# Optimization experiments

Measured on AMD Instinct MI355X. Metric: run time of the kernel, lower is better.

Reference implementation:

```python
import jax, jax.numpy as jnp
import numpy as np

B, H = 1, 512
NVAR, NCLS = 16384, 65536
NP, NM = 4096, 4096
NEG = -1e30


def setup_inputs() -> dict:
    key = jax.random.key(0)
    ks = jax.random.split(key, 16)
    s = 0.02  # weight init scale
    return {
        "literal_emb": jax.random.normal(ks[0], (B, 2 * NVAR, H), jnp.float32),
        "clause_emb": jax.random.normal(ks[1], (B, NCLS, H), jnp.float32),
        "pos_idx": jax.random.randint(ks[2], (NP,), 0, NCLS),
        "neg_idx": jax.random.randint(ks[3], (NM,), 0, NCLS),
        "keep_mask": jax.random.randint(ks[4], (NP, NM), 0, 2).astype(bool),
        "taken_mask": jax.random.uniform(ks[5], (NP, NM)) < 0.01,  # sparse exclusion set
        "var_K_w": s * jax.random.normal(ks[6], (H, H), jnp.float32),
        "var_K_b": jnp.zeros((H,), jnp.float32),
        "var_Q_w": s * jax.random.normal(ks[7], (H, H), jnp.float32),
        "var_Q_b": jnp.zeros((H,), jnp.float32),
        "var_attn_w": s * jax.random.normal(ks[8], (1, H), jnp.float32),
        "var_attn_b": jnp.zeros((1,), jnp.float32),
        "W_Q_w": s * jax.random.normal(ks[9], (H, H), jnp.float32),
        "W_Q_b": jnp.zeros((H,), jnp.float32),
        "W_K_w": s * jax.random.normal(ks[10], (H, H), jnp.float32),
        "W_K_b": jnp.zeros((H,), jnp.float32),
    }


def reference(literal_emb, clause_emb, pos_idx, neg_idx, keep_mask, taken_mask,
              var_K_w, var_K_b, var_Q_w, var_Q_b, var_attn_w, var_attn_b,
              W_Q_w, W_Q_b, W_K_w, W_K_b):
    n_vars = literal_emb.shape[1] // 2
    # --- select_var: additive attention over positive literals ---
    K = literal_emb[:, :n_vars]                       # [B, V, H]
    K_t = K @ var_K_w.T + var_K_b                     # [B, V, H]
    Q = clause_emb.sum(axis=1)                        # [B, H] (C_aggr='sum')
    Q_t = Q @ var_Q_w.T + var_Q_b                     # [B, H]
    u = (jnp.tanh(K_t + Q_t[:, None, :]) @ var_attn_w.T + var_attn_b)[..., 0]  # [B, V]
    log_score = jax.nn.log_softmax(u, axis=-1)
    var_logp = jnp.max(log_score, axis=-1)            # [B]
    var_idx = jnp.argmax(log_score, axis=-1)          # [B]
    # --- clause-pair attention over pivot pos/neg clause pools ---
    q = clause_emb[:, pos_idx] @ W_Q_w.T + W_Q_b      # [B, NP, H]
    k = clause_emb[:, neg_idx] @ W_K_w.T + W_K_b      # [B, NM, H]
    h = q.shape[-1]
    scores = jnp.einsum('bnh,bmh->bnm', q, k) / jnp.sqrt(jnp.float32(h))
    # mask_grid_asym: drop invalid (keep_mask==0) and already-taken pairs, log-normalize
    valid = keep_mask & (~taken_mask)                 # [NP, NM]
    masked = jnp.where(valid[None], scores, jnp.float32(NEG))
    flat = masked.reshape(masked.shape[0], -1)        # [B, NP*NM]
    logp = jax.nn.log_softmax(flat, axis=-1)
    C_logp = jnp.max(logp, axis=-1)                   # [B]
    C_flat = jnp.argmax(logp, axis=-1)                # [B]
    M = scores.shape[-1]
    ci, cj = C_flat // M, C_flat % M
    c_idx_pos = pos_idx[ci]                           # map back to global clause ids
    c_idx_neg = neg_idx[cj]
    c_logp = C_logp + var_logp                        # [B]
    return (c_logp, c_idx_pos, c_idx_neg, var_idx)
```

## Files before the change

### kernel.cpp

```cpp
#include <hip/hip_runtime.h>
#include <hip/hip_bf16.h>
#include <math.h>

#define HH 512
#define NVARS 16384
#define NPOS 4096
#define NMS 4096
#define NEGV -1.0e30f
#define RSQRT_H 0.04419417382415922f

#define BM 128
#define BK 16

typedef unsigned short u16;
typedef __attribute__((ext_vector_type(8))) short bf16x8;
typedef __attribute__((ext_vector_type(4))) float f32x4;

struct SPart { float m; float s; int a; int pad; };

__device__ inline u16 f2bf(float f) {
  unsigned u = __float_as_uint(f);
  unsigned r = (u + 0x7fffu + ((u >> 16) & 1u)) >> 16;
  return (u16)r;
}
__device__ inline float bf2f(u16 h) { return __uint_as_float(((unsigned)h) << 16); }

__device__ inline void wreduce_maxidx(float& v, int& idx) {
#pragma unroll
  for (int m = 1; m < 64; m <<= 1) {
    float ov = __shfl_xor(v, m, 64);
    int oi = __shfl_xor(idx, m, 64);
    if (ov > v || (ov == v && oi < idx)) { v = ov; idx = oi; }
  }
}

__device__ inline float wreduce_sum(float v) {
#pragma unroll
  for (int m = 1; m < 64; m <<= 1) v += __shfl_xor(v, m, 64);
  return v;
}

__device__ __forceinline__ void stage_frag(const u16* src, u16* dst) {
  __builtin_amdgcn_global_load_lds(
      (const __attribute__((address_space(1))) void*)src,
      (__attribute__((address_space(3))) void*)dst, 16, 0, 0);
}

__global__ __launch_bounds__(256) void pack_kernel(
    const void* __restrict__ keep, const void* __restrict__ taken,
    unsigned long long* __restrict__ vmask) {
  __shared__ unsigned char nib[256];
  const unsigned* kw = (const unsigned*)keep;
  int f = 1;
#pragma unroll
  for (int i = 0; i < 16; ++i) f &= (kw[i] <= 1u);
  const int t = threadIdx.x;
  const size_t e = (size_t)blockIdx.x * 1024 + (size_t)t * 4;
  int v0, v1, v2, v3;
  if (f) {
    uint4 kv = *(const uint4*)((const unsigned int*)keep + e);
    uint4 tv = *(const uint4*)((const unsigned int*)taken + e);
    v0 = kv.x && !tv.x; v1 = kv.y && !tv.y; v2 = kv.z && !tv.z; v3 = kv.w && !tv.w;
  } else {
    unsigned kv = *(const unsigned*)((const unsigned char*)keep + e);
    unsigned tv = *(const unsigned*)((const unsigned char*)taken + e);
    v0 = (kv & 0xffu) && !(tv & 0xffu);
    v1 = (kv & 0xff00u) && !(tv & 0xff00u);
    v2 = (kv & 0xff0000u) && !(tv & 0xff0000u);
    v3 = (kv & 0xff000000u) && !(tv & 0xff000000u);
  }
  nib[t] = (unsigned char)(v0 | (v1 << 1) | (v2 << 2) | (v3 << 3));
  __syncthreads();
  if (t < 16) {
    unsigned long long m = 0;
#pragma unroll
    for (int j = 0; j < 16; ++j)
      m |= (unsigned long long)nib[t * 16 + j] << (4 * j);
    vmask[(size_t)blockIdx.x * 16 + t] = m;
  }
}

__global__ __launch_bounds__(256) void qsum_kernel(
    const float* __restrict__ clause, double* __restrict__ qpart) {
  const int b = blockIdx.x, t = threadIdx.x;
  const int fg = t & 127;
  const int rh = t >> 7;
  const float* base = clause + (size_t)(b * 128 + rh * 64) * HH + fg * 4;
  double a0 = 0.0, a1 = 0.0, a2 = 0.0, a3 = 0.0;
#pragma unroll 4
  for (int r = 0; r < 64; ++r) {
    float4 v = *(const float4*)(base + (size_t)r * HH);
    a0 += (double)v.x; a1 += (double)v.y; a2 += (double)v.z; a3 += (double)v.w;
  }
  double* o = qpart + (size_t)(b * 2 + rh) * HH + fg * 4;
  o[0] = a0; o[1] = a1; o[2] = a2; o[3] = a3;
}

__global__ __launch_bounds__(256) void qred_kernel(
    const double* __restrict__ qpart, double* __restrict__ Qd) {
  __shared__ double red[256];
  const int t = threadIdx.x;
  const int h = blockIdx.x * 16 + (t & 15);
  const int chunk = t >> 4;
  double s = 0.0;
  for (int j = 0; j < 64; ++j) s += qpart[(size_t)(chunk * 64 + j) * HH + h];
  red[t] = s;
  __syncthreads();
  for (int off = 8; off > 0; off >>= 1) {
    if (chunk < off) red[t] += red[t + off * 16];
    __syncthreads();
  }
  if (t < 16) Qd[blockIdx.x * 16 + t] = red[t];
}

__global__ __launch_bounds__(256) void prepmv_kernel(
    const double* __restrict__ Qd, const float* __restrict__ varQw,
    const float* __restrict__ varQb, const float* __restrict__ varKb,
    float* __restrict__ tvec) {
  __shared__ double red[256];
  const int t = threadIdx.x;
  const int h = blockIdx.x * 16 + (t & 15);
  const int chunk = t >> 4;
  const float* wrow = varQw + (size_t)h * HH + chunk * 32;
  const double* qd = Qd + chunk * 32;
  double s = 0.0;
  for (int j = 0; j < 32; ++j) s += qd[j] * (double)wrow[j];
  red[t] = s;
  __syncthreads();
  for (int off = 8; off > 0; off >>= 1) {
    if (chunk < off) red[t] += red[t + off * 16];
    __syncthreads();
  }
  if (t < 16) {
    int hh = blockIdx.x * 16 + t;
    tvec[hh] = (float)(red[t] + (double)varQb[hh] + (double)varKb[hh]);
  }
}

__global__ __launch_bounds__(256) void tofrag_kernel(
    const float* __restrict__ src, u16* __restrict__ hi, u16* __restrict__ lo) {
  const int frag = blockIdx.x * 4 + (threadIdx.x >> 6);
  const int lane = threadIdx.x & 63;
  const int R = frag >> 4, K = frag & 15;
  const float* p = src + (size_t)(R * 16 + (lane & 15)) * HH + K * 32 + (lane >> 4) * 8;
  float v[8];
  *(float4*)&v[0] = *(const float4*)p;
  *(float4*)&v[4] = *(const float4*)(p + 4);
  u16 h[8], l[8];
#pragma unroll
  for (int e = 0; e < 8; ++e) { h[e] = f2bf(v[e]); l[e] = f2bf(v[e] - bf2f(h[e])); }
  size_t base = (size_t)frag * 512 + (size_t)lane * 8;
  *(ushort4*)(hi + base) = *(ushort4*)&h[0];
  *(ushort4*)(hi + base + 4) = *(ushort4*)&h[4];
  *(ushort4*)(lo + base) = *(ushort4*)&l[0];
  *(ushort4*)(lo + base + 4) = *(ushort4*)&l[4];
}

#define MFMA16(A, B)                                                                 \
  _Pragma("unroll") for (int i_ = 0; i_ < 4; ++i_)                                   \
  _Pragma("unroll") for (int j_ = 0; j_ < 4; ++j_)                                   \
    acc[i_][j_] = __builtin_amdgcn_mfma_f32_16x16x32_bf16(A[i_], B[j_], acc[i_][j_], 0, 0, 0);

#define MFMAS(AH, AL, BH, BL)                                                        \
  do { MFMA16(AH, BH) MFMA16(AH, BL) MFMA16(AL, BH) } while (0)

__global__ __launch_bounds__(256, 3) void proj_kernel(
    const float* __restrict__ clause,
    const int* __restrict__ pos_idx, const int* __restrict__ neg_idx,
    const u16* __restrict__ wqhi, const u16* __restrict__ wqlo,
    const u16* __restrict__ wkhi2, const u16* __restrict__ wklo2,
    const float* __restrict__ bQ, const float* __restrict__ bK,
    float* __restrict__ qmat, float* __restrict__ kmat) {
  const int* __restrict__ idx = blockIdx.z ? neg_idx : pos_idx;
  const u16* __restrict__ bhp = blockIdx.z ? wkhi2 : wqhi;
  const u16* __restrict__ blp = blockIdx.z ? wklo2 : wqlo;
  const float* __restrict__ bias = blockIdx.z ? bK : bQ;
  float* __restrict__ out = blockIdx.z ? kmat : qmat;

  const int t = threadIdx.x, lane = t & 63, wid = t >> 6;
  const int wn = wid & 1, wm = wid >> 1;
  const int row0 = blockIdx.x * 128;
  const int col0 = blockIdx.y * 128;

  const float* aptr[4];
#pragma unroll
  for (int f = 0; f < 4; ++f) {
    int g = idx[row0 + wn * 64 + f * 16 + (lane & 15)];
    aptr[f] = clause + (size_t)g * HH + (lane >> 4) * 8;
  }
  const size_t bbase = (size_t)((col0 >> 4) + wm * 4) * 8192 + (size_t)lane * 8;

  f32x4 acc[4][4] = {};
#pragma unroll
  for (int s = 0; s < 16; ++s) {
    float rA[4][8];
    bf16x8 aH[4], aL[4], bH[4], bL[4];
#pragma unroll
    for (int f = 0; f < 4; ++f) {
      *(float4*)&rA[f][0] = *(const float4*)(aptr[f] + s * 32);
      *(float4*)&rA[f][4] = *(const float4*)(aptr[f] + s * 32 + 4);
      size_t ob = bbase + (size_t)f * 8192 + (size_t)s * 512;
      bH[f] = *(const bf16x8*)(bhp + ob);
      bL[f] = *(const bf16x8*)(blp + ob);
    }
#pragma unroll
    for (int f = 0; f < 4; ++f)
#pragma unroll
      for (int e = 0; e < 8; ++e) {
        float v = rA[f][e];
        u16 h = f2bf(v);
        aH[f][e] = (short)h;
        aL[f][e] = (short)f2bf(v - bf2f(h));
      }
    MFMAS(aH, aL, bH, bL);
  }

#pragma unroll
  for (int i = 0; i < 4; ++i)
#pragma unroll
    for (int j = 0; j < 4; ++j) {
      int h = col0 + wm * 64 + j * 16 + (lane & 15);
      float b = bias[h];
#pragma unroll
      for (int r = 0; r < 4; ++r) {
        int n = row0 + wn * 64 + i * 16 + (lane >> 4) * 4 + r;
        out[(size_t)n * HH + h] = acc[i][j][r] + b;
      }
    }
}


__global__ __launch_bounds__(256, 2) void ktu_kernel(
    const u16* __restrict__ lithi, const u16* __restrict__ litlo,
    const u16* __restrict__ wkhi, const u16* __restrict__ wklo,
    const float* __restrict__ tvec, const float* __restrict__ attnw,
    float* __restrict__ upart) {
  __shared__ __align__(16) u16 lds[2][4][8][512];
  const int t = threadIdx.x, lane = t & 63, wid = t >> 6;
  const int wn = wid & 1, wm = wid >> 1;
  const int row0 = blockIdx.x * 128;
  const int l8 = lane * 8;

  const u16* sa = (wid == 0) ? lithi : (wid == 1) ? litlo : (wid == 2) ? wkhi : wklo;
  const int rb = (wid < 2) ? (row0 >> 4) : (blockIdx.y * 8);
  const u16* sab = sa + (size_t)rb * 8192 + l8;

#define KSTAGE(buf, s)                                                        \
  _Pragma("unroll") for (int f_ = 0; f_ < 8; ++f_)                            \
    stage_frag(sab + (size_t)f_ * 8192 + (size_t)(s) * 512,                   \
               &lds[buf][wid][f_][0]);

  KSTAGE(0, 0)
  f32x4 acc[4][4] = {};
#pragma unroll
  for (int s = 0; s < 16; ++s) {
    __syncthreads();
    if (s < 15) { KSTAGE((s + 1) & 1, s + 1) }
    const int b = s & 1;
    bf16x8 aH[4], aL[4], bH[4], bL[4];
#pragma unroll
    for (int f = 0; f < 4; ++f) {
      aH[f] = *(const bf16x8*)&lds[b][0][wn * 4 + f][l8];
      aL[f] = *(const bf16x8*)&lds[b][1][wn * 4 + f][l8];
      bH[f] = *(const bf16x8*)&lds[b][2][wm * 4 + f][l8];
      bL[f] = *(const bf16x8*)&lds[b][3][wm * 4 + f][l8];
    }
    MFMAS(aH, aL, bH, bL);
  }
#undef KSTAGE

  const int cbase = blockIdx.y * 128 + wm * 64;
  float tv[4], aw[4];
#pragma unroll
  for (int j = 0; j < 4; ++j) {
    int c = cbase + j * 16 + (lane & 15);
    tv[j] = tvec[c]; aw[j] = attnw[c];
  }
  float us[4][4];
#pragma unroll
  for (int i = 0; i < 4; ++i)
#pragma unroll
    for (int r = 0; r < 4; ++r) {
      float s = 0.f;
#pragma unroll
      for (int j = 0; j < 4; ++j) {
        float x = acc[i][j][r] + tv[j];
        float th = 1.0f - 2.0f / (__expf(2.0f * x) + 1.0f);
        s += th * aw[j];
      }
      us[i][r] = s;
    }
#pragma unroll
  for (int m = 1; m < 16; m <<= 1)
#pragma unroll
    for (int i = 0; i < 4; ++i)
#pragma unroll
      for (int r = 0; r < 4; ++r) us[i][r] += __shfl_xor(us[i][r], m, 64);
  if ((lane & 15) == 0) {
#pragma unroll
    for (int i = 0; i < 4; ++i)
#pragma unroll
      for (int r = 0; r < 4; ++r) {
        int row = row0 + wn * 64 + i * 16 + (lane >> 4) * 4 + r;
        upart[(size_t)(blockIdx.y * 2 + wm) * NVARS + row] = us[i][r];
      }
  }
}

__global__ __launch_bounds__(256, 2) void scores_kernel(
    const u16* __restrict__ qhi, const u16* __restrict__ qlo,
    const u16* __restrict__ khi, const u16* __restrict__ klo,
    const unsigned long long* __restrict__ vmask, SPart* __restrict__ parts) {
  __shared__ __align__(16) u16 lds[2][4][8][512];
  __shared__ unsigned long long mrow[128][2];
  __shared__ float s_rv[4]; __shared__ int s_ri[4]; __shared__ float s_rs[4];
  __shared__ float s_bm; __shared__ int s_ba;

  const int t = threadIdx.x;
  const int lane = t & 63;
  const int wid = t >> 6;
  const int wn = wid & 1, wm = wid >> 1;
  const int l8 = lane * 8;

  const int bid = blockIdx.x;
  const int xcd = bid & 7, p = bid >> 3;
  const int sp = p >> 6, q = p & 63;
  const int g = xcd * 2 + sp;
  const int bx = (g & 3) * 8 + (q & 7);
  const int by = (g >> 2) * 8 + (q >> 3);

  const int n0 = by * 128;
  const int m0 = bx * 128;

  const u16* sa = (wid == 0) ? qhi : (wid == 1) ? qlo : (wid == 2) ? khi : klo;
  const int rb = (wid < 2) ? (n0 >> 4) : (m0 >> 4);
  const u16* sab = sa + (size_t)rb * 8192 + l8;

#define SSTAGE(buf, s)                                                        \
  _Pragma("unroll") for (int f_ = 0; f_ < 8; ++f_)                            \
    stage_frag(sab + (size_t)f_ * 8192 + (size_t)(s) * 512,                   \
               &lds[buf][wid][f_][0]);

  {
    int r = t >> 1, w = t & 1;
    mrow[r][w] = vmask[(size_t)(n0 + r) * (NMS / 64) + (m0 >> 6) + w];
  }

  SSTAGE(0, 0)
  f32x4 acc[4][4] = {};
#pragma unroll
  for (int s = 0; s < 16; ++s) {
    __syncthreads();
    if (s < 15) { SSTAGE((s + 1) & 1, s + 1) }
    const int b = s & 1;
    bf16x8 aH[4], aL[4], bH[4], bL[4];
#pragma unroll
    for (int f = 0; f < 4; ++f) {
      aH[f] = *(const bf16x8*)&lds[b][0][wn * 4 + f][l8];
      aL[f] = *(const bf16x8*)&lds[b][1][wn * 4 + f][l8];
      bH[f] = *(const bf16x8*)&lds[b][2][wm * 4 + f][l8];
      bL[f] = *(const bf16x8*)&lds[b][3][wm * 4 + f][l8];
    }
    MFMAS(aH, aL, bH, bL);
  }
#undef SSTAGE

  const int rbase = wn * 64 + (lane >> 4) * 4;
  const int cb15 = (lane & 15);

  float mv = NEGV; int mi = 0x7fffffff;
#pragma unroll
  for (int i = 0; i < 4; ++i) {
#pragma unroll
    for (int r = 0; r < 4; ++r) {
      int rl = rbase + i * 16 + r;
      unsigned long long ww = mrow[rl][wm];
      int gb = (n0 + rl) * NMS + m0;
#pragma unroll
      for (int j = 0; j < 4; ++j) {
        int bit = j * 16 + cb15;
        int cl = wm * 64 + bit;
        float sv = acc[i][j][r] * RSQRT_H;
        acc[i][j][r] = sv;
        bool valid = ((ww >> bit) & 1ull) != 0;
        if (valid && (sv > mv || (sv == mv && gb + cl < mi))) { mv = sv; mi = gb + cl; }
      }
    }
  }
  wreduce_maxidx(mv, mi);
  if ((t & 63) == 0) { s_rv[wid] = mv; s_ri[wid] = mi; }
  __syncthreads();
  if (t == 0) {
    float bm = s_rv[0]; int ba = s_ri[0];
    for (int w = 1; w < 4; ++w)
      if (s_rv[w] > bm || (s_rv[w] == bm && s_ri[w] < ba)) { bm = s_rv[w]; ba = s_ri[w]; }
    s_bm = bm; s_ba = ba;
  }
  __syncthreads();
  const float bm = s_bm;

  float se = 0.f;
#pragma unroll
  for (int i = 0; i < 4; ++i) {
#pragma unroll
    for (int r = 0; r < 4; ++r) {
      int rl = rbase + i * 16 + r;
      unsigned long long ww = mrow[rl][wm];
#pragma unroll
      for (int j = 0; j < 4; ++j) {
        int bit = j * 16 + cb15;
        bool valid = ((ww >> bit) & 1ull) != 0;
        if (valid) se += __expf(acc[i][j][r] - bm);
      }
    }
  }
  se = wreduce_sum(se);
  if ((t & 63) == 0) s_rs[wid] = se;
  __syncthreads();
  if (t == 0) {
    SPart pt;
    pt.m = s_bm;
    pt.s = s_rs[0] + s_rs[1] + s_rs[2] + s_rs[3];
    pt.a = s_ba; pt.pad = 0;
    parts[by * 32 + bx] = pt;
  }
}

__global__ __launch_bounds__(256) void usum_kernel(
    const float* __restrict__ upart, SPart* __restrict__ uparts2) {
  __shared__ float s_rv[4]; __shared__ int s_ri[4]; __shared__ float s_rs[4];
  __shared__ float s_bm; __shared__ int s_ba;
  const int t = threadIdx.x;
  const int i = blockIdx.x * 256 + t;
  float u = 0.f;
#pragma unroll
  for (int p = 0; p < 8; ++p) u += upart[(size_t)p * NVARS + i];
  float mv = u; int mi = i;
  wreduce_maxidx(mv, mi);
  if ((t & 63) == 0) { s_rv[t >> 6] = mv; s_ri[t >> 6] = mi; }
  __syncthreads();
  if (t == 0) {
    float bm = s_rv[0]; int ba = s_ri[0];
    for (int w = 1; w < 4; ++w)
      if (s_rv[w] > bm || (s_rv[w] == bm && s_ri[w] < ba)) { bm = s_rv[w]; ba = s_ri[w]; }
    s_bm = bm; s_ba = ba;
  }
  __syncthreads();
  float se = __expf(u - s_bm);
  se = wreduce_sum(se);
  if ((t & 63) == 0) s_rs[t >> 6] = se;
  __syncthreads();
  if (t == 0) {
    SPart p;
    p.m = s_bm;
    p.s = s_rs[0] + s_rs[1] + s_rs[2] + s_rs[3];
    p.a = s_ba; p.pad = 0;
    uparts2[blockIdx.x] = p;
  }
}

__global__ __launch_bounds__(256) void final_kernel(
    const SPart* __restrict__ uparts2, const SPart* __restrict__ parts,
    const int* __restrict__ pos_idx, const int* __restrict__ neg_idx,
    float* __restrict__ out) {
  __shared__ float s_rv[4]; __shared__ int s_ri[4]; __shared__ float s_rs[4];
  __shared__ float s_umax; __shared__ int s_uarg; __shared__ float s_usum;
  __shared__ float s_gm; __shared__ int s_ga;
  const int t = threadIdx.x;

  float mv = -3.0e38f; int mi = 0x7fffffff;
  SPart up;
  if (t < 64) {
    up = uparts2[t];
    mv = up.m; mi = up.a;
  }
  wreduce_maxidx(mv, mi);
  if ((t & 63) == 0) { s_rv[t >> 6] = mv; s_ri[t >> 6] = mi; }
  __syncthreads();
  if (t == 0) {
    float bm = s_rv[0]; int ba = s_ri[0];
    for (int w = 1; w < 4; ++w)
      if (s_rv[w] > bm || (s_rv[w] == bm && s_ri[w] < ba)) { bm = s_rv[w]; ba = s_ri[w]; }
    s_umax = bm; s_uarg = ba;
  }
  __syncthreads();
  float se = (t < 64) ? up.s * __expf(up.m - s_umax) : 0.f;
  se = wreduce_sum(se);
  if ((t & 63) == 0) s_rs[t >> 6] = se;
  __syncthreads();
  if (t == 0) s_usum = s_rs[0] + s_rs[1] + s_rs[2] + s_rs[3];
  __syncthreads();

  mv = NEGV; mi = 0x7fffffff;
  for (int i = t; i < 1024; i += 256) {
    SPart p = parts[i];
    if (p.m > mv || (p.m == mv && p.a < mi)) { mv = p.m; mi = p.a; }
  }
  wreduce_maxidx(mv, mi);
  if ((t & 63) == 0) { s_rv[t >> 6] = mv; s_ri[t >> 6] = mi; }
  __syncthreads();
  if (t == 0) {
    float bm = s_rv[0]; int ba = s_ri[0];
    for (int w = 1; w < 4; ++w)
      if (s_rv[w] > bm || (s_rv[w] == bm && s_ri[w] < ba)) { bm = s_rv[w]; ba = s_ri[w]; }
    s_gm = bm; s_ga = ba;
  }
  __syncthreads();
  const float gm = s_gm;
  float ss = 0.f;
  for (int i = t; i < 1024; i += 256) {
    SPart p = parts[i];
    ss += p.s * __expf(p.m - gm);
  }
  ss = wreduce_sum(ss);
  if ((t & 63) == 0) s_rs[t >> 6] = ss;
  __syncthreads();
  if (t == 0) {
    float gsum = s_rs[0] + s_rs[1] + s_rs[2] + s_rs[3];
    float c_logp = -logf(gsum) - logf(s_usum);
    int ga = s_ga;
    if (ga == 0x7fffffff) ga = 0;
    int ci = ga >> 12, cj = ga & 4095;
    out[0] = c_logp;
    out[1] = (float)pos_idx[ci];
    out[2] = (float)neg_idx[cj];
    out[3] = (float)s_uarg;
  }
}

extern "C" void kernel_launch(void* const* d_in, const int* in_sizes, int n_in,
                              void* d_out, int out_size, void* d_ws, size_t ws_size,
                              hipStream_t stream) {
  (void)in_sizes; (void)n_in; (void)out_size; (void)ws_size;
  const float* lit    = (const float*)d_in[0];
  const float* clause = (const float*)d_in[1];
  const int* pos_idx  = (const int*)d_in[2];
  const int* neg_idx  = (const int*)d_in[3];
  const void* keep    = d_in[4];
  const void* taken   = d_in[5];
  const float* varKw  = (const float*)d_in[6];
  const float* varKb  = (const float*)d_in[7];
  const float* varQw  = (const float*)d_in[8];
  const float* varQb  = (const float*)d_in[9];
  const float* attnw  = (const float*)d_in[10];
  const float* WQw    = (const float*)d_in[12];
  const float* WQb    = (const float*)d_in[13];
  const float* WKw    = (const float*)d_in[14];
  const float* WKb    = (const float*)d_in[15];

  char* ws = (char*)d_ws;
  size_t off = 0;
  auto alloc = [&](size_t b) {
    char* p = ws + off;
    off = (off + b + 255) & ~(size_t)255;
    return p;
  };
  double* qpart              = (double*)alloc((size_t)1024 * HH * 8);
  double* Qd                 = (double*)alloc(HH * 8);
  float* tvec                = (float*)alloc(HH * 4);
  float* upart               = (float*)alloc(8 * (size_t)NVARS * 4);
  unsigned long long* vmask  = (unsigned long long*)alloc((size_t)NPOS * (NMS / 64) * 8);
  float* qmat                = (float*)alloc((size_t)NPOS * HH * 4);
  float* kmat                = (float*)alloc((size_t)NMS * HH * 4);
  u16* qhi                   = (u16*)alloc((size_t)NPOS * HH * 2);
  u16* qlo                   = (u16*)alloc((size_t)NPOS * HH * 2);
  u16* khi                   = (u16*)alloc((size_t)NMS * HH * 2);
  u16* klo                   = (u16*)alloc((size_t)NMS * HH * 2);
  u16* wkhi                  = (u16*)alloc((size_t)HH * HH * 2);
  u16* wklo                  = (u16*)alloc((size_t)HH * HH * 2);
  u16* pwqhi                 = (u16*)alloc((size_t)HH * HH * 2);
  u16* pwqlo                 = (u16*)alloc((size_t)HH * HH * 2);
  u16* pwkhi                 = (u16*)alloc((size_t)HH * HH * 2);
  u16* pwklo                 = (u16*)alloc((size_t)HH * HH * 2);
  u16* lithi                 = (u16*)alloc((size_t)NVARS * HH * 2);
  u16* litlo                 = (u16*)alloc((size_t)NVARS * HH * 2);
  SPart* parts               = (SPart*)alloc(1024 * sizeof(SPart));
  SPart* uparts2             = (SPart*)alloc(64 * sizeof(SPart));

  pack_kernel<<<16384, 256, 0, stream>>>(keep, taken, vmask);
  qsum_kernel<<<512, 256, 0, stream>>>(clause, qpart);
  qred_kernel<<<32, 256, 0, stream>>>(qpart, Qd);
  prepmv_kernel<<<32, 256, 0, stream>>>(Qd, varQw, varQb, varKb, tvec);
  tofrag_kernel<<<128, 256, 0, stream>>>(varKw, wkhi, wklo);
  tofrag_kernel<<<128, 256, 0, stream>>>(WQw, pwqhi, pwqlo);
  tofrag_kernel<<<128, 256, 0, stream>>>(WKw, pwkhi, pwklo);
  tofrag_kernel<<<4096, 256, 0, stream>>>(lit, lithi, litlo);
  proj_kernel<<<dim3(32, 4, 2), 256, 0, stream>>>(clause, pos_idx, neg_idx,
                                                  pwqhi, pwqlo, pwkhi, pwklo,
                                                  WQb, WKb, qmat, kmat);
  tofrag_kernel<<<1024, 256, 0, stream>>>(qmat, qhi, qlo);
  tofrag_kernel<<<1024, 256, 0, stream>>>(kmat, khi, klo);
  ktu_kernel<<<dim3(128, 4), 256, 0, stream>>>(lithi, litlo, wkhi, wklo,
                                               tvec, attnw, upart);
  scores_kernel<<<1024, 256, 0, stream>>>(qhi, qlo, khi, klo, vmask, parts);
  usum_kernel<<<64, 256, 0, stream>>>(upart, uparts2);
  final_kernel<<<1, 256, 0, stream>>>(uparts2, parts, pos_idx, neg_idx,
                                      (float*)d_out);
}
```

Measured before the change: 222.0 us.

## Merge prep kernels into one launch and emit bf16 hi/lo fragments from projection

Merges the mask packing, clause-sum partials and all weight/literal fragment conversions into a single multi-role prep kernel, which cuts several launches. The projection kernel swaps its operand roles so its accumulator layout can be written straight into the MFMA fragment layout as bf16 hi/lo pairs with bias added. This removes the fp32 q/k intermediates and the two tofrag passes over them. The cost is a more complex store-index mapping and a large heterogeneous grid whose blocks vary in cost.

```diff
diff --git a/kernel.cpp b/kernel.cpp
--- a/kernel.cpp
+++ b/kernel.cpp
@@ -9,9 +9,6 @@
 #define NEGV -1.0e30f
 #define RSQRT_H 0.04419417382415922f
 
-#define BM 128
-#define BK 16
-
 typedef unsigned short u16;
 typedef __attribute__((ext_vector_type(8))) short bf16x8;
 typedef __attribute__((ext_vector_type(4))) float f32x4;
@@ -46,54 +43,88 @@
       (__attribute__((address_space(3))) void*)dst, 16, 0, 0);
 }
 
-__global__ __launch_bounds__(256) void pack_kernel(
+__device__ __forceinline__ void do_tofrag(
+    const float* __restrict__ src, u16* __restrict__ hi, u16* __restrict__ lo,
+    int frag, int lane) {
+  const int R = frag >> 4, K = frag & 15;
+  const float* p = src + (size_t)(R * 16 + (lane & 15)) * HH + K * 32 + (lane >> 4) * 8;
+  float v[8];
+  *(float4*)&v[0] = *(const float4*)p;
+  *(float4*)&v[4] = *(const float4*)(p + 4);
+  u16 h[8], l[8];
+#pragma unroll
+  for (int e = 0; e < 8; ++e) { h[e] = f2bf(v[e]); l[e] = f2bf(v[e] - bf2f(h[e])); }
+  size_t base = (size_t)frag * 512 + (size_t)lane * 8;
+  *(ushort4*)(hi + base) = *(ushort4*)&h[0];
+  *(ushort4*)(hi + base + 4) = *(ushort4*)&h[4];
+  *(ushort4*)(lo + base) = *(ushort4*)&l[0];
+  *(ushort4*)(lo + base + 4) = *(ushort4*)&l[4];
+}
+
+__global__ __launch_bounds__(256) void prep_kernel(
     const void* __restrict__ keep, const void* __restrict__ taken,
-    unsigned long long* __restrict__ vmask) {
-  __shared__ unsigned char nib[256];
-  const unsigned* kw = (const unsigned*)keep;
-  int f = 1;
-#pragma unroll
-  for (int i = 0; i < 16; ++i) f &= (kw[i] <= 1u);
+    unsigned long long* __restrict__ vmask,
+    const float* __restrict__ clause, double* __restrict__ qpart,
+    const float* __restrict__ lit, u16* __restrict__ lithi, u16* __restrict__ litlo,
+    const float* __restrict__ varKw, u16* __restrict__ wkhi, u16* __restrict__ wklo,
+    const float* __restrict__ WQw, u16* __restrict__ pwqhi, u16* __restrict__ pwqlo,
+    const float* __restrict__ WKw, u16* __restrict__ pwkhi, u16* __restrict__ pwklo) {
+  const int bid = blockIdx.x;
   const int t = threadIdx.x;
-  const size_t e = (size_t)blockIdx.x * 1024 + (size_t)t * 4;
-  int v0, v1, v2, v3;
-  if (f) {
-    uint4 kv = *(const uint4*)((const unsigned int*)keep + e);
-    uint4 tv = *(const uint4*)((const unsigned int*)taken + e);
-    v0 = kv.x && !tv.x; v1 = kv.y && !tv.y; v2 = kv.z && !tv.z; v3 = kv.w && !tv.w;
+  if (bid < 16384) {
+    __shared__ unsigned char nib[256];
+    const unsigned* kw = (const unsigned*)keep;
+    int f = 1;
+#pragma unroll
+    for (int i = 0; i < 16; ++i) f &= (kw[i] <= 1u);
+    const size_t e = (size_t)bid * 1024 + (size_t)t * 4;
+    int v0, v1, v2, v3;
+    if (f) {
+      uint4 kv = *(const uint4*)((const unsigned int*)keep + e);
+      uint4 tv = *(const uint4*)((const unsigned int*)taken + e);
+      v0 = kv.x && !tv.x; v1 = kv.y && !tv.y; v2 = kv.z && !tv.z; v3 = kv.w && !tv.w;
+    } else {
+      unsigned kv = *(const unsigned*)((const unsigned char*)keep + e);
+      unsigned tv = *(const unsigned*)((const unsigned char*)taken + e);
+      v0 = (kv & 0xffu) && !(tv & 0xffu);
+      v1 = (kv & 0xff00u) && !(tv & 0xff00u);
+      v2 = (kv & 0xff0000u) && !(tv & 0xff0000u);
+      v3 = (kv & 0xff000000u) && !(tv & 0xff000000u);
+    }
+    nib[t] = (unsigned char)(v0 | (v1 << 1) | (v2 << 2) | (v3 << 3));
+    __syncthreads();
+    if (t < 16) {
+      unsigned long long m = 0;
+#pragma unroll
+      for (int j = 0; j < 16; ++j)
+        m |= (unsigned long long)nib[t * 16 + j] << (4 * j);
+      vmask[(size_t)bid * 16 + t] = m;
+    }
+  } else if (bid < 16896) {
+    const int b = bid - 16384;
+    const int fg = t & 127;
+    const int rh = t >> 7;
+    const float* base = clause + (size_t)(b * 128 + rh * 64) * HH + fg * 4;
+    double a0 = 0.0, a1 = 0.0, a2 = 0.0, a3 = 0.0;
+#pragma unroll 4
+    for (int r = 0; r < 64; ++r) {
+      float4 v = *(const float4*)(base + (size_t)r * HH);
+      a0 += (double)v.x; a1 += (double)v.y; a2 += (double)v.z; a3 += (double)v.w;
+    }
+    double* o = qpart + (size_t)(b * 2 + rh) * HH + fg * 4;
+    o[0] = a0; o[1] = a1; o[2] = a2; o[3] = a3;
+  } else if (bid < 20992) {
+    const int frag = (bid - 16896) * 4 + (t >> 6);
+    do_tofrag(lit, lithi, litlo, frag, t & 63);
   } else {
-    unsigned kv = *(const unsigned*)((const unsigned char*)keep + e);
-    unsigned tv = *(const unsigned*)((const unsigned char*)taken + e);
-    v0 = (kv & 0xffu) && !(tv & 0xffu);
-    v1 = (kv & 0xff00u) && !(tv & 0xff00u);
-    v2 = (kv & 0xff0000u) && !(tv & 0xff0000u);
-    v3 = (kv & 0xff000000u) && !(tv & 0xff000000u);
-  }
-  nib[t] = (unsigned char)(v0 | (v1 << 1) | (v2 << 2) | (v3 << 3));
-  __syncthreads();
-  if (t < 16) {
-    unsigned long long m = 0;
-#pragma unroll
-    for (int j = 0; j < 16; ++j)
-      m |= (unsigned long long)nib[t * 16 + j] << (4 * j);
-    vmask[(size_t)blockIdx.x * 16 + t] = m;
-  }
-}
-
-__global__ __launch_bounds__(256) void qsum_kernel(
-    const float* __restrict__ clause, double* __restrict__ qpart) {
-  const int b = blockIdx.x, t = threadIdx.x;
-  const int fg = t & 127;
-  const int rh = t >> 7;
-  const float* base = clause + (size_t)(b * 128 + rh * 64) * HH + fg * 4;
-  double a0 = 0.0, a1 = 0.0, a2 = 0.0, a3 = 0.0;
-#pragma unroll 4
-  for (int r = 0; r < 64; ++r) {
-    float4 v = *(const float4*)(base + (size_t)r * HH);
-    a0 += (double)v.x; a1 += (double)v.y; a2 += (double)v.z; a3 += (double)v.w;
-  }
-  double* o = qpart + (size_t)(b * 2 + rh) * HH + fg * 4;
-  o[0] = a0; o[1] = a1; o[2] = a2; o[3] = a3;
+    const int wb = bid - 20992;
+    const int m = wb >> 7;
+    const int frag = (wb & 127) * 4 + (t >> 6);
+    const float* src = (m == 0) ? varKw : (m == 1) ? WQw : WKw;
+    u16* hi = (m == 0) ? wkhi : (m == 1) ? pwqhi : pwkhi;
+    u16* lo = (m == 0) ? wklo : (m == 1) ? pwqlo : pwklo;
+    do_tofrag(src, hi, lo, frag, t & 63);
+  }
 }
 
 __global__ __launch_bounds__(256) void qred_kernel(
@@ -137,25 +168,6 @@
   }
 }
 
-__global__ __launch_bounds__(256) void tofrag_kernel(
-    const float* __restrict__ src, u16* __restrict__ hi, u16* __restrict__ lo) {
-  const int frag = blockIdx.x * 4 + (threadIdx.x >> 6);
-  const int lane = threadIdx.x & 63;
-  const int R = frag >> 4, K = frag & 15;
-  const float* p = src + (size_t)(R * 16 + (lane & 15)) * HH + K * 32 + (lane >> 4) * 8;
-  float v[8];
-  *(float4*)&v[0] = *(const float4*)p;
-  *(float4*)&v[4] = *(const float4*)(p + 4);
-  u16 h[8], l[8];
-#pragma unroll
-  for (int e = 0; e < 8; ++e) { h[e] = f2bf(v[e]); l[e] = f2bf(v[e] - bf2f(h[e])); }
-  size_t base = (size_t)frag * 512 + (size_t)lane * 8;
-  *(ushort4*)(hi + base) = *(ushort4*)&h[0];
-  *(ushort4*)(hi + base + 4) = *(ushort4*)&h[4];
-  *(ushort4*)(lo + base) = *(ushort4*)&l[0];
-  *(ushort4*)(lo + base + 4) = *(ushort4*)&l[4];
-}
-
 #define MFMA16(A, B)                                                                 \
   _Pragma("unroll") for (int i_ = 0; i_ < 4; ++i_)                                   \
   _Pragma("unroll") for (int j_ = 0; j_ < 4; ++j_)                                   \
@@ -167,68 +179,82 @@
 __global__ __launch_bounds__(256, 3) void proj_kernel(
     const float* __restrict__ clause,
     const int* __restrict__ pos_idx, const int* __restrict__ neg_idx,
-    const u16* __restrict__ wqhi, const u16* __restrict__ wqlo,
-    const u16* __restrict__ wkhi2, const u16* __restrict__ wklo2,
+    const u16* __restrict__ pwqhi, const u16* __restrict__ pwqlo,
+    const u16* __restrict__ pwkhi, const u16* __restrict__ pwklo,
     const float* __restrict__ bQ, const float* __restrict__ bK,
-    float* __restrict__ qmat, float* __restrict__ kmat) {
+    u16* __restrict__ qhi, u16* __restrict__ qlo,
+    u16* __restrict__ khi, u16* __restrict__ klo) {
   const int* __restrict__ idx = blockIdx.z ? neg_idx : pos_idx;
-  const u16* __restrict__ bhp = blockIdx.z ? wkhi2 : wqhi;
-  const u16* __restrict__ blp = blockIdx.z ? wklo2 : wqlo;
+  const u16* __restrict__ whp = blockIdx.z ? pwkhi : pwqhi;
+  const u16* __restrict__ wlp = blockIdx.z ? pwklo : pwqlo;
   const float* __restrict__ bias = blockIdx.z ? bK : bQ;
-  float* __restrict__ out = blockIdx.z ? kmat : qmat;
+  u16* __restrict__ ohi = blockIdx.z ? khi : qhi;
+  u16* __restrict__ olo = blockIdx.z ? klo : qlo;
 
   const int t = threadIdx.x, lane = t & 63, wid = t >> 6;
   const int wn = wid & 1, wm = wid >> 1;
   const int row0 = blockIdx.x * 128;
   const int col0 = blockIdx.y * 128;
 
-  const float* aptr[4];
-#pragma unroll
-  for (int f = 0; f < 4; ++f) {
-    int g = idx[row0 + wn * 64 + f * 16 + (lane & 15)];
-    aptr[f] = clause + (size_t)g * HH + (lane >> 4) * 8;
-  }
-  const size_t bbase = (size_t)((col0 >> 4) + wm * 4) * 8192 + (size_t)lane * 8;
+  const float* bptr[4];
+#pragma unroll
+  for (int j = 0; j < 4; ++j) {
+    int g = idx[row0 + wn * 64 + j * 16 + (lane & 15)];
+    bptr[j] = clause + (size_t)g * HH + (lane >> 4) * 8;
+  }
+  const size_t abase = (size_t)((col0 >> 4) + wm * 4) * 8192 + (size_t)lane * 8;
 
   f32x4 acc[4][4] = {};
 #pragma unroll
   for (int s = 0; s < 16; ++s) {
-    float rA[4][8];
+    float rB[4][8];
     bf16x8 aH[4], aL[4], bH[4], bL[4];
 #pragma unroll
     for (int f = 0; f < 4; ++f) {
-      *(float4*)&rA[f][0] = *(const float4*)(aptr[f] + s * 32);
-      *(float4*)&rA[f][4] = *(const float4*)(aptr[f] + s * 32 + 4);
-      size_t ob = bbase + (size_t)f * 8192 + (size_t)s * 512;
-      bH[f] = *(const bf16x8*)(bhp + ob);
-      bL[f] = *(const bf16x8*)(blp + ob);
+      *(float4*)&rB[f][0] = *(const float4*)(bptr[f] + s * 32);
+      *(float4*)&rB[f][4] = *(const float4*)(bptr[f] + s * 32 + 4);
+      size_t oa = abase + (size_t)f * 8192 + (size_t)s * 512;
+      aH[f] = *(const bf16x8*)(whp + oa);
+      aL[f] = *(const bf16x8*)(wlp + oa);
     }
 #pragma unroll
     for (int f = 0; f < 4; ++f)
 #pragma unroll
       for (int e = 0; e < 8; ++e) {
-        float v = rA[f][e];
+        float v = rB[f][e];
         u16 h = f2bf(v);
-        aH[f][e] = (short)h;
-        aL[f][e] = (short)f2bf(v - bf2f(h));
+        bH[f][e] = (short)h;
+        bL[f][e] = (short)f2bf(v - bf2f(h));
       }
-    MFMAS(aH, aL, bH, bL);
-  }
-
-#pragma unroll
-  for (int i = 0; i < 4; ++i)
+    MFMA16(aH, bH)
+    MFMA16(aL, bH)
+    MFMA16(aH, bL)
+  }
+
+  const int q4 = lane >> 4;
+#pragma unroll
+  for (int i = 0; i < 4; ++i) {
+    const int hbase = col0 + wm * 64 + i * 16 + q4 * 4;
+    float b0 = bias[hbase + 0], b1 = bias[hbase + 1];
+    float b2 = bias[hbase + 2], b3 = bias[hbase + 3];
+    const int lane16 = (lane & 15) + ((i & 1) * 2 + (q4 >> 1)) * 16;
+    const int sub = (q4 & 1) * 4;
 #pragma unroll
     for (int j = 0; j < 4; ++j) {
-      int h = col0 + wm * 64 + j * 16 + (lane & 15);
-      float b = bias[h];
-#pragma unroll
-      for (int r = 0; r < 4; ++r) {
-        int n = row0 + wn * 64 + i * 16 + (lane >> 4) * 4 + r;
-        out[(size_t)n * HH + h] = acc[i][j][r] + b;
-      }
-    }
-}
-
+      const int frag = ((row0 + wn * 64 + j * 16) >> 4) * 16 +
+                       ((col0 + wm * 64 + i * 16) >> 5);
+      size_t base = (size_t)frag * 512 + (size_t)lane16 * 8 + sub;
+      ushort4 hv, lv;
+      float v;
+      v = acc[i][j][0] + b0; hv.x = f2bf(v); lv.x = f2bf(v - bf2f(hv.x));
+      v = acc[i][j][1] + b1; hv.y = f2bf(v); lv.y = f2bf(v - bf2f(hv.y));
+      v = acc[i][j][2] + b2; hv.z = f2bf(v); lv.z = f2bf(v - bf2f(hv.z));
+      v = acc[i][j][3] + b3; hv.w = f2bf(v); lv.w = f2bf(v - bf2f(hv.w));
+      *(ushort4*)(ohi + base) = hv;
+      *(ushort4*)(olo + base) = lv;
+    }
+  }
+}
 
 __global__ __launch_bounds__(256, 2) void ktu_kernel(
     const u16* __restrict__ lithi, const u16* __restrict__ litlo,
@@ -560,8 +586,6 @@
   float* tvec                = (float*)alloc(HH * 4);
   float* upart               = (float*)alloc(8 * (size_t)NVARS * 4);
   unsigned long long* vmask  = (unsigned long long*)alloc((size_t)NPOS * (NMS / 64) * 8);
-  float* qmat                = (float*)alloc((size_t)NPOS * HH * 4);
-  float* kmat                = (float*)alloc((size_t)NMS * HH * 4);
   u16* qhi                   = (u16*)alloc((size_t)NPOS * HH * 2);
   u16* qlo                   = (u16*)alloc((size_t)NPOS * HH * 2);
   u16* khi                   = (u16*)alloc((size_t)NMS * HH * 2);
@@ -577,19 +601,17 @@
   SPart* parts               = (SPart*)alloc(1024 * sizeof(SPart));
   SPart* uparts2             = (SPart*)alloc(64 * sizeof(SPart));
 
-  pack_kernel<<<16384, 256, 0, stream>>>(keep, taken, vmask);
-  qsum_kernel<<<512, 256, 0, stream>>>(clause, qpart);
+  prep_kernel<<<21376, 256, 0, stream>>>(keep, taken, vmask, clause, qpart,
+                                         lit, lithi, litlo,
+                                         varKw, wkhi, wklo,
+                                         WQw, pwqhi, pwqlo,
+                                         WKw, pwkhi, pwklo);
   qred_kernel<<<32, 256, 0, stream>>>(qpart, Qd);
   prepmv_kernel<<<32, 256, 0, stream>>>(Qd, varQw, varQb, varKb, tvec);
-  tofrag_kernel<<<128, 256, 0, stream>>>(varKw, wkhi, wklo);
-  tofrag_kernel<<<128, 256, 0, stream>>>(WQw, pwqhi, pwqlo);
-  tofrag_kernel<<<128, 256, 0, stream>>>(WKw, pwkhi, pwklo);
-  tofrag_kernel<<<4096, 256, 0, stream>>>(lit, lithi, litlo);
   proj_kernel<<<dim3(32, 4, 2), 256, 0, stream>>>(clause, pos_idx, neg_idx,
                                                   pwqhi, pwqlo, pwkhi, pwklo,
-                                                  WQb, WKb, qmat, kmat);
-  tofrag_kernel<<<1024, 256, 0, stream>>>(qmat, qhi, qlo);
-  tofrag_kernel<<<1024, 256, 0, stream>>>(kmat, khi, klo);
+                                                  WQb, WKb,
+                                                  qhi, qlo, khi, klo);
   ktu_kernel<<<dim3(128, 4), 256, 0, stream>>>(lithi, litlo, wkhi, wklo,
                                                tvec, attnw, upart);
   scores_kernel<<<1024, 256, 0, stream>>>(qhi, qlo, khi, klo, vmask, parts);
```

Measured after the change: 217.4 us. 2.1% less time.
